# Performance work log

Measured on AMD Instinct MI355X. Metric: run time of the kernel, lower is better.

Reference implementation:

```python
import jax, jax.numpy as jnp
import numpy as np

N = 50000      # n_nodes
E = 800000     # n_edges (avg degree 16)
IN, HID, CLS = 128, 128, 40


def setup_inputs() -> dict:
    key = jax.random.key(0)
    ks = jax.random.split(key, 9)
    features = jax.random.normal(ks[0], (N, IN), dtype=jnp.float32)
    src = jax.random.randint(ks[1], (E,), 0, N)
    dst = jax.random.randint(ks[2], (E,), 0, N)
    # GraphConv weights (glorot-ish scale) and biases
    W0 = jax.random.normal(ks[3], (IN, HID), dtype=jnp.float32) / np.sqrt(IN).astype(np.float32)
    b0 = jnp.zeros((HID,), jnp.float32)
    W1 = jax.random.normal(ks[4], (HID, HID), dtype=jnp.float32) / np.sqrt(HID).astype(np.float32)
    b1 = jnp.zeros((HID,), jnp.float32)
    W2 = jax.random.normal(ks[5], (HID, CLS), dtype=jnp.float32) / np.sqrt(HID).astype(np.float32)
    b2 = jnp.zeros((CLS,), jnp.float32)
    return {"features": features, "src": src, "dst": dst,
            "W0": W0, "b0": b0, "W1": W1, "b1": b1, "W2": W2, "b2": b2}


def _degree_norms(src, dst, dtype):
    # DGL GraphConv norm='both': D_out^{-1/2} on source side, D_in^{-1/2} on dest side,
    # degrees clamped to a minimum of 1.
    ones = jnp.ones(src.shape[0], dtype)
    deg_out = jax.ops.segment_sum(ones, src, num_segments=N)
    deg_in = jax.ops.segment_sum(ones, dst, num_segments=N)
    norm_out = jnp.where(deg_out > 0, deg_out, 1.0) ** -0.5
    norm_in = jnp.where(deg_in > 0, deg_in, 1.0) ** -0.5
    return norm_out, norm_in


def _graph_conv(h, src, dst, norm_out, norm_in, W, b, act):
    # h' = D_in^{-1/2} A D_out^{-1/2} h W + b ; optional relu
    h = (h * norm_out[:, None]) @ W            # dense transform first (in >= out)
    agg = jax.ops.segment_sum(h[src], dst, num_segments=N)  # sparse aggregation
    out = agg * norm_in[:, None] + b
    return jax.nn.relu(out) if act else out


def reference(features, src, dst, W0, b0, W1, b1, W2, b2):
    norm_out, norm_in = _degree_norms(src, dst, features.dtype)
    # dropout is identity in eval mode
    h = _graph_conv(features, src, dst, norm_out, norm_in, W0, b0, True)
    h = _graph_conv(h, src, dst, norm_out, norm_in, W1, b1, True)
    h = _graph_conv(h, src, dst, norm_out, norm_in, W2, b2, False)
    return h
```

## Files before the change

kernel.cpp:

```cpp
#include <hip/hip_runtime.h>
#include <hip/hip_fp16.h>


static constexpr int NN  = 50000;
static constexpr int NE  = 800000;
static constexpr int HID = 128;
static constexpr int CLS = 40;
static constexpr int CAP = 48;

static constexpr int NGEMM  = (NN + 127) / 128;
static constexpr int NBUILD = (NE + 1023) / 1024;
static constexpr int NPREP1 = 8;
static constexpr int NPREP2 = 3;

typedef __attribute__((ext_vector_type(8))) _Float16 f16x8;
typedef __attribute__((ext_vector_type(4))) float    f32x4;
union ABu { uint4 u; f16x8 h; };

__device__ __forceinline__ void gemm128_body(const float* __restrict__ X,
                                             const float* __restrict__ W,
                                             __half* __restrict__ Y,
                                             int tileIdx, float* As, float* Bs) {
    constexpr int BSTR = 132;
    const int tid = threadIdx.x;
    const int rowBase = tileIdx * 128;

    const int bkk = tid >> 3;
    const int bc4 = tid & 7;
    const float* wrow = W + (size_t)bkk * 128 + bc4 * 16;

    const int rt = tid & 15;
    const int ct = tid >> 4;

    float acc[8][8];
    #pragma unroll
    for (int j = 0; j < 8; ++j)
        #pragma unroll
        for (int i = 0; i < 8; ++i) acc[j][i] = 0.f;

    float4 xv[4], wv[4];

    auto loadA = [&](int s) {
        #pragma unroll
        for (int i = 0; i < 4; ++i) {
            int f = tid + 256 * i;
            int r = f >> 3;
            int kc = f & 7;
            int grow = rowBase + r;
            xv[i] = (grow < NN)
                ? *(const float4*)(X + (size_t)grow * 128 + s * 32 + kc * 4)
                : make_float4(0.f, 0.f, 0.f, 0.f);
        }
    };
    auto loadB = [&](int s) {
        const float* p = wrow + (size_t)s * 32 * 128;
        #pragma unroll
        for (int i = 0; i < 4; ++i) wv[i] = ((const float4*)p)[i];
    };
    auto writeLDS = [&]() {
        #pragma unroll
        for (int i = 0; i < 4; ++i) {
            int f = tid + 256 * i;
            int r = f >> 3;
            int kc = f & 7;
            int pc = ((r >> 2) + kc) & 31;
            int base = pc * 4 + (r & 3);
            const float* v = (const float*)&xv[i];
            #pragma unroll
            for (int c = 0; c < 4; ++c)
                As[(kc * 4 + c) * 128 + base] = v[c];
        }
        #pragma unroll
        for (int i = 0; i < 4; ++i)
            *(float4*)&Bs[bkk * BSTR + bc4 * 16 + i * 4] = wv[i];
    };

    loadA(0); loadB(0);
    for (int s = 0; s < 4; ++s) {
        writeLDS();
        __syncthreads();
        if (s < 3) { loadA(s + 1); loadB(s + 1); }
        #pragma unroll 8
        for (int k = 0; k < 32; ++k) {
            int kc = k >> 2;
            int pa0 = (rt + kc) & 31;
            int pa1 = (rt + 16 + kc) & 31;
            float4 a0 = *(const float4*)&As[k * 128 + pa0 * 4];
            float4 a1 = *(const float4*)&As[k * 128 + pa1 * 4];
            float4 b0 = *(const float4*)&Bs[k * BSTR + ct * 8];
            float4 b1 = *(const float4*)&Bs[k * BSTR + ct * 8 + 4];
            float a[8] = {a0.x, a0.y, a0.z, a0.w, a1.x, a1.y, a1.z, a1.w};
            float b[8] = {b0.x, b0.y, b0.z, b0.w, b1.x, b1.y, b1.z, b1.w};
            #pragma unroll
            for (int j = 0; j < 8; ++j)
                #pragma unroll
                for (int ii = 0; ii < 8; ++ii)
                    acc[j][ii] = fmaf(a[j], b[ii], acc[j][ii]);
        }
        __syncthreads();
    }
    union Pack { __half2 h2[4]; uint4 u; };
    #pragma unroll
    for (int j = 0; j < 8; ++j) {
        int row = rowBase + ((j < 4) ? (4 * rt + j) : (64 + 4 * rt + (j - 4)));
        if (row < NN) {
            Pack p;
            #pragma unroll
            for (int q = 0; q < 4; ++q)
                p.h2[q] = __halves2half2(__float2half_rn(acc[j][2 * q]),
                                         __float2half_rn(acc[j][2 * q + 1]));
            *(uint4*)(Y + (size_t)row * 128 + ct * 8) = p.u;
        }
    }
}

__global__ __launch_bounds__(256) void fused_kernel(const float* __restrict__ X,
                                                    const float* __restrict__ W0,
                                                    __half* __restrict__ Y,
                                                    const int* __restrict__ src,
                                                    const int* __restrict__ dst,
                                                    int* __restrict__ deg_out,
                                                    int* __restrict__ cnt,
                                                    unsigned short* __restrict__ colbkt,
                                                    const float* __restrict__ W1,
                                                    __half* __restrict__ W1t,
                                                    const float* __restrict__ W2,
                                                    __half* __restrict__ W2t) {
    __shared__ float As[32 * 128];
    __shared__ float Bs[32 * 132];
    int b = blockIdx.x;
    if (b < NGEMM) {
        gemm128_body(X, W0, Y, b, As, Bs);
    } else if (b < NGEMM + NBUILD) {
        int base = (b - NGEMM) * 1024 + threadIdx.x;
        int e[4], s[4], d[4];
        #pragma unroll
        for (int i = 0; i < 4; ++i) {
            e[i] = base + 256 * i;
            int ec = e[i] < NE ? e[i] : NE - 1;
            s[i] = src[ec];
            d[i] = dst[ec];
        }
        #pragma unroll
        for (int i = 0; i < 4; ++i)
            if (e[i] < NE) atomicAdd(&deg_out[s[i]], 1);
        int slot[4];
        #pragma unroll
        for (int i = 0; i < 4; ++i)
            slot[i] = (e[i] < NE) ? atomicAdd(&cnt[d[i]], 1) : CAP;
        #pragma unroll
        for (int i = 0; i < 4; ++i)
            if (slot[i] < CAP)
                colbkt[(size_t)d[i] * CAP + slot[i]] = (unsigned short)s[i];
    } else if (b < NGEMM + NBUILD + NPREP1) {
        int gid = (b - NGEMM - NBUILD) * 256 + threadIdx.x;
        int n = gid >> 4, q = gid & 15;
        union { __half h[8]; uint4 u; } p;
        #pragma unroll
        for (int j = 0; j < 8; ++j)
            p.h[j] = __float2half_rn(W1[(size_t)(q * 8 + j) * 128 + n]);
        ((uint4*)W1t)[n * 16 + ((q + n) & 15)] = p.u;
    } else {
        int gid = (b - NGEMM - NBUILD - NPREP1) * 256 + threadIdx.x;
        int n = gid >> 4, q = gid & 15;
        union { __half h[8]; uint4 u; } p;
        #pragma unroll
        for (int j = 0; j < 8; ++j)
            p.h[j] = (n < CLS) ? __float2half_rn(W2[(size_t)(q * 8 + j) * CLS + n])
                               : __half(0.f);
        ((uint4*)W2t)[n * 16 + ((q + n) & 15)] = p.u;
    }
}

template <int NT>
__device__ __forceinline__ void mfma_rowgemm_body(const __half* __restrict__ H,
                                                  const float* __restrict__ norm_out,
                                                  __half* __restrict__ Y,
                                                  const __half* Ws) {
    const int tid  = threadIdx.x;
    const int wv   = tid >> 6;
    const int lane = tid & 63;
    const int m    = lane & 15;
    const int quad = lane >> 4;
    const int rowW = blockIdx.x * 64 + wv * 16;

    ABu a[4];
    int arow = rowW + m;
    if (arow >= NN) arow = NN - 1;
    const uint4* hp = (const uint4*)(H + (size_t)arow * 128);
    #pragma unroll
    for (int kc = 0; kc < 4; ++kc)
        a[kc].u = hp[kc * 4 + quad];

    __syncthreads();

    f32x4 acc[NT];
    #pragma unroll
    for (int nt = 0; nt < NT; ++nt) acc[nt] = (f32x4){0.f, 0.f, 0.f, 0.f};

    #pragma unroll
    for (int kc = 0; kc < 4; ++kc) {
        #pragma unroll
        for (int nt = 0; nt < NT; ++nt) {
            int n = nt * 16 + m;
            int q = kc * 4 + quad;
            ABu bf;
            bf.u = ((const uint4*)Ws)[n * 16 + ((q + n) & 15)];
            acc[nt] = __builtin_amdgcn_mfma_f32_16x16x32_f16(a[kc].h, bf.h, acc[nt], 0, 0, 0);
        }
    }

    float nmv[4];
    #pragma unroll
    for (int r = 0; r < 4; ++r) {
        int row = rowW + quad * 4 + r;
        nmv[r] = (row < NN) ? norm_out[row] : 0.f;
    }
    #pragma unroll
    for (int nt = 0; nt < NT; ++nt) {
        int coln = nt * 16 + m;
        #pragma unroll
        for (int r = 0; r < 4; ++r) {
            int row = rowW + quad * 4 + r;
            if (row < NN)
                Y[(size_t)row * (NT * 16) + coln] = __float2half_rn(acc[nt][r] * nmv[r]);
        }
    }
}

__global__ __launch_bounds__(256) void gemm1_mfma(const __half* __restrict__ H,
                                                  const __half* __restrict__ W1t,
                                                  const float* __restrict__ norm_out,
                                                  __half* __restrict__ T) {
    __shared__ __half Ws[128 * 128];
    const int tid = threadIdx.x;
    #pragma unroll
    for (int i = 0; i < 8; ++i)
        ((uint4*)Ws)[tid + 256 * i] = ((const uint4*)W1t)[tid + 256 * i];
    mfma_rowgemm_body<8>(H, norm_out, T, Ws);
}

__global__ __launch_bounds__(256) void gemm40_mfma(const __half* __restrict__ H,
                                                   const __half* __restrict__ W2t,
                                                   const float* __restrict__ norm_out,
                                                   __half* __restrict__ T40) {
    __shared__ __half Ws[48 * 128];
    const int tid = threadIdx.x;
    #pragma unroll
    for (int i = 0; i < 3; ++i)
        ((uint4*)Ws)[tid + 256 * i] = ((const uint4*)W2t)[tid + 256 * i];
    mfma_rowgemm_body<3>(H, norm_out, T40, Ws);
}

__global__ __launch_bounds__(256) void norm_scale_kernel(const int* __restrict__ deg_out,
                                                         const int* __restrict__ cnt,
                                                         float* __restrict__ norm_out,
                                                         float* __restrict__ norm_in,
                                                         __half* __restrict__ t) {
    __shared__ float nms[32];
    int base = blockIdx.x * 32;
    int tid = threadIdx.x;
    if (tid < 32) {
        int v = base + tid;
        float no = 1.f;
        if (v < NN) {
            int dof = deg_out[v], dif = cnt[v];
            no = rsqrtf((float)(dof > 0 ? dof : 1));
            norm_out[v] = no;
            norm_in[v]  = rsqrtf((float)(dif > 0 ? dif : 1));
        }
        nms[tid] = no;
    }
    __syncthreads();
    for (int i = tid; i < 512; i += 256) {
        int ro = i >> 4, ch = i & 15;
        int v = base + ro;
        if (v < NN) {
            uint4* p = (uint4*)t + (size_t)v * 16 + ch;
            uint4 u = *p;
            float nm = nms[ro];
            __half2* hp = (__half2*)&u;
            #pragma unroll
            for (int q = 0; q < 4; ++q) {
                float2 f = __half22float2(hp[q]);
                hp[q] = __halves2half2(__float2half_rn(f.x * nm),
                                       __float2half_rn(f.y * nm));
            }
            *p = u;
        }
    }
}

__global__ __launch_bounds__(256) void agg128h_kernel(const __half* __restrict__ T,
                                                      const unsigned short* __restrict__ colbkt,
                                                      const int* __restrict__ cnt,
                                                      const float* __restrict__ norm_in,
                                                      const float* __restrict__ bias,
                                                      __half* __restrict__ out) {
    const int wv   = threadIdx.x >> 6;
    const int lane = threadIdx.x & 63;
    const int nodeA = blockIdx.x * 8 + wv * 2;
    const int nodeB = nodeA + 1;
    if (nodeA >= NN) return;
    const int grp = lane >> 4;
    const int l16 = lane & 15;

    int dgA = cnt[nodeA]; if (dgA > CAP) dgA = CAP;
    int dgB = (nodeB < NN) ? cnt[nodeB] : 0; if (dgB > CAP) dgB = CAP;
    const unsigned short* bktA = colbkt + (size_t)nodeA * CAP;
    const unsigned short* bktB = colbkt + (size_t)(nodeB < NN ? nodeB : 0) * CAP;

    float accA[8], accB[8];
    #pragma unroll
    for (int i = 0; i < 8; ++i) { accA[i] = 0.f; accB[i] = 0.f; }

    const int dgM = dgA > dgB ? dgA : dgB;
    for (int j = 0; j < dgM; j += 16) {
        uint4 vA[4], vB[4];
        float wA[4], wB[4];
        #pragma unroll
        for (int u = 0; u < 4; ++u) {
            int e   = j + 4 * u + grp;
            int eA  = e < dgA ? e : 0;   wA[u] = e < dgA ? 1.f : 0.f;
            int eB  = e < dgB ? e : 0;   wB[u] = e < dgB ? 1.f : 0.f;
            int sA  = (int)bktA[eA];
            int sB  = (int)bktB[eB];
            vA[u] = ((const uint4*)(T + (size_t)sA * 128))[l16];
            vB[u] = ((const uint4*)(T + (size_t)sB * 128))[l16];
        }
        #pragma unroll
        for (int u = 0; u < 4; ++u) {
            const __half2* ha = (const __half2*)&vA[u];
            const __half2* hb = (const __half2*)&vB[u];
            #pragma unroll
            for (int q = 0; q < 4; ++q) {
                float2 fa = __half22float2(ha[q]);
                float2 fb = __half22float2(hb[q]);
                accA[2 * q]     = fmaf(fa.x, wA[u], accA[2 * q]);
                accA[2 * q + 1] = fmaf(fa.y, wA[u], accA[2 * q + 1]);
                accB[2 * q]     = fmaf(fb.x, wB[u], accB[2 * q]);
                accB[2 * q + 1] = fmaf(fb.y, wB[u], accB[2 * q + 1]);
            }
        }
    }
    #pragma unroll
    for (int i = 0; i < 8; ++i) {
        accA[i] += __shfl_xor(accA[i], 16, 64);
        accA[i] += __shfl_xor(accA[i], 32, 64);
        accB[i] += __shfl_xor(accB[i], 16, 64);
        accB[i] += __shfl_xor(accB[i], 32, 64);
    }
    if (grp < 2) {
        int node = (grp == 0) ? nodeA : nodeB;
        const float* ac = (grp == 0) ? accA : accB;
        if (node < NN) {
            float nm = norm_in[node];
            float4 b0 = ((const float4*)bias)[l16 * 2];
            float4 b1 = ((const float4*)bias)[l16 * 2 + 1];
            float o[8];
            o[0] = fmaf(ac[0], nm, b0.x); o[1] = fmaf(ac[1], nm, b0.y);
            o[2] = fmaf(ac[2], nm, b0.z); o[3] = fmaf(ac[3], nm, b0.w);
            o[4] = fmaf(ac[4], nm, b1.x); o[5] = fmaf(ac[5], nm, b1.y);
            o[6] = fmaf(ac[6], nm, b1.z); o[7] = fmaf(ac[7], nm, b1.w);
            union { __half2 h2[4]; uint4 u; } pk;
            #pragma unroll
            for (int q = 0; q < 4; ++q) {
                float x = fmaxf(o[2 * q], 0.f);
                float y = fmaxf(o[2 * q + 1], 0.f);
                pk.h2[q] = __halves2half2(__float2half_rn(x), __float2half_rn(y));
            }
            ((uint4*)(out + (size_t)node * 128))[l16] = pk.u;
        }
    }
}

__global__ __launch_bounds__(256) void agg40h_kernel(const __half* __restrict__ T,
                                                     const unsigned short* __restrict__ colbkt,
                                                     const int* __restrict__ cnt,
                                                     const float* __restrict__ norm_in,
                                                     const float* __restrict__ bias,
                                                     float* __restrict__ out) {
    int node = blockIdx.x * 4 + (threadIdx.x >> 6);
    int lane = threadIdx.x & 63;
    if (node >= NN) return;
    int dg = cnt[node];
    if (dg > CAP) dg = CAP;
    const unsigned short* bkt = colbkt + (size_t)node * CAP;
    const int g = lane / 6;
    const int c = lane - g * 6;

    float acc[8];
    #pragma unroll
    for (int i = 0; i < 8; ++i) acc[i] = 0.f;

    constexpr int B = 4;
    for (int j = 0; j < dg; j += 8 * B) {
        uint4 v[B];
        float w[B];
        #pragma unroll
        for (int u = 0; u < B; ++u) {
            int e  = j + 8 * u + g;
            bool p = (g < 8) && (e < dg);
            int ec = p ? e : 0;
            int s  = (int)bkt[ec];
            w[u]   = p ? 1.f : 0.f;
            v[u]   = ((const uint4*)(T + (size_t)s * 48))[c];
        }
        #pragma unroll
        for (int u = 0; u < B; ++u) {
            const __half2* hp = (const __half2*)&v[u];
            #pragma unroll
            for (int q = 0; q < 4; ++q) {
                float2 f = __half22float2(hp[q]);
                acc[2 * q]     = fmaf(f.x, w[u], acc[2 * q]);
                acc[2 * q + 1] = fmaf(f.y, w[u], acc[2 * q + 1]);
            }
        }
    }
    #pragma unroll
    for (int i = 0; i < 8; ++i) {
        acc[i] += __shfl(acc[i], lane + 24, 64);
        acc[i] += __shfl(acc[i], lane + 12, 64);
        acc[i] += __shfl(acc[i], lane + 6, 64);
    }
    if (lane < 5) {
        float nm = norm_in[node];
        float4 o0, o1;
        o0.x = fmaf(acc[0], nm, bias[c * 8 + 0]);
        o0.y = fmaf(acc[1], nm, bias[c * 8 + 1]);
        o0.z = fmaf(acc[2], nm, bias[c * 8 + 2]);
        o0.w = fmaf(acc[3], nm, bias[c * 8 + 3]);
        o1.x = fmaf(acc[4], nm, bias[c * 8 + 4]);
        o1.y = fmaf(acc[5], nm, bias[c * 8 + 5]);
        o1.z = fmaf(acc[6], nm, bias[c * 8 + 6]);
        o1.w = fmaf(acc[7], nm, bias[c * 8 + 7]);
        float* op = out + (size_t)node * 40 + c * 8;
        *(float4*)op       = o0;
        *(float4*)(op + 4) = o1;
    }
}

extern "C" void kernel_launch(void* const* d_in, const int* in_sizes, int n_in,
                              void* d_out, int out_size, void* d_ws, size_t ws_size,
                              hipStream_t stream) {
    const float* features = (const float*)d_in[0];
    const int*   src      = (const int*)d_in[1];
    const int*   dst      = (const int*)d_in[2];
    const float* W0       = (const float*)d_in[3];
    const float* b0       = (const float*)d_in[4];
    const float* W1       = (const float*)d_in[5];
    const float* b1       = (const float*)d_in[6];
    const float* W2       = (const float*)d_in[7];
    const float* b2       = (const float*)d_in[8];
    float*       out      = (float*)d_out;

    char* ws = (char*)d_ws;
    auto alloc = [&](size_t bytes) {
        char* p = ws;
        ws += (bytes + 511) & ~(size_t)511;
        return p;
    };
    int*            deg_out  = (int*)alloc((size_t)NN * 4);
    int*            cnt      = (int*)alloc((size_t)NN * 4);
    float*          norm_out = (float*)alloc((size_t)NN * 4);
    float*          norm_in  = (float*)alloc((size_t)NN * 4);
    unsigned short* colbkt   = (unsigned short*)alloc((size_t)NN * CAP * 2);
    __half*         W1t      = (__half*)alloc((size_t)HID * HID * 2);
    __half*         W2t      = (__half*)alloc((size_t)48 * HID * 2);
    __half*         t        = (__half*)alloc((size_t)NN * HID * 2);
    __half*         h        = (__half*)alloc((size_t)NN * HID * 2);
    __half*         t40      = (__half*)alloc((size_t)NN * 48 * 2);
    if ((size_t)(ws - (char*)d_ws) > ws_size) return;

    hipMemsetAsync(deg_out, 0, (size_t)NN * 4, stream);
    hipMemsetAsync(cnt, 0, (size_t)NN * 4, stream);

    int gAgg2  = (NN + 7) / 8;
    int gAgg   = (NN + 3) / 4;
    int gRow64 = (NN + 63) / 64;

    fused_kernel<<<NGEMM + NBUILD + NPREP1 + NPREP2, 256, 0, stream>>>(
        features, W0, t, src, dst, deg_out, cnt, colbkt, W1, W1t, W2, W2t);
    norm_scale_kernel<<<(NN + 31) / 32, 256, 0, stream>>>(deg_out, cnt, norm_out, norm_in, t);

    agg128h_kernel<<<gAgg2, 256, 0, stream>>>(t, colbkt, cnt, norm_in, b0, h);
    gemm1_mfma<<<gRow64, 256, 0, stream>>>(h, W1t, norm_out, t);
    agg128h_kernel<<<gAgg2, 256, 0, stream>>>(t, colbkt, cnt, norm_in, b1, h);
    gemm40_mfma<<<gRow64, 256, 0, stream>>>(h, W2t, norm_out, t40);
    agg40h_kernel<<<gAgg, 256, 0, stream>>>(t40, colbkt, cnt, norm_in, b2, out);
}
```

Baseline: 265.1 us.

## Split 128-wide aggregation into four 32-column phases for cache locality

The 128-feature aggregation kernel is split into four column phases, each launched as its own block range and gathering only a 32-half (64-byte) slice of each source row. The aim is for each phase's working set (50000 rows x 64 B, about 3.2 MB) to stay resident in L2/LLC, so the random neighbour gathers hit cache instead of going to HBM. In exchange, index and count loads are repeated four times, each lane issues one load per iteration instead of four, and the cross-lane reduction needs two extra shuffle stages.

New measurement: 344.5 us. 29.9% more time.

```diff
diff --git a/kernel.cpp b/kernel.cpp
--- a/kernel.cpp
+++ b/kernel.cpp
@@ -12,6 +12,7 @@
 static constexpr int NBUILD = (NE + 1023) / 1024;
 static constexpr int NPREP1 = 8;
 static constexpr int NPREP2 = 3;
+static constexpr int BPP    = (NN + 7) / 8;
 
 typedef __attribute__((ext_vector_type(8))) _Float16 f16x8;
 typedef __attribute__((ext_vector_type(4))) float    f32x4;
@@ -291,24 +292,27 @@
     }
 }
 
-__global__ __launch_bounds__(256) void agg128h_kernel(const __half* __restrict__ T,
+__global__ __launch_bounds__(256) void agg128p_kernel(const __half* __restrict__ T,
                                                       const unsigned short* __restrict__ colbkt,
                                                       const int* __restrict__ cnt,
                                                       const float* __restrict__ norm_in,
                                                       const float* __restrict__ bias,
                                                       __half* __restrict__ out) {
-    const int wv   = threadIdx.x >> 6;
-    const int lane = threadIdx.x & 63;
-    const int nodeA = blockIdx.x * 8 + wv * 2;
+    const int phase = blockIdx.x / BPP;
+    const int bip   = blockIdx.x - phase * BPP;
+    const int wv    = threadIdx.x >> 6;
+    const int lane  = threadIdx.x & 63;
+    const int e     = lane >> 2;
+    const int c     = lane & 3;
+    const int nodeA = (bip * 4 + wv) * 2;
     const int nodeB = nodeA + 1;
     if (nodeA >= NN) return;
-    const int grp = lane >> 4;
-    const int l16 = lane & 15;
 
     int dgA = cnt[nodeA]; if (dgA > CAP) dgA = CAP;
     int dgB = (nodeB < NN) ? cnt[nodeB] : 0; if (dgB > CAP) dgB = CAP;
     const unsigned short* bktA = colbkt + (size_t)nodeA * CAP;
     const unsigned short* bktB = colbkt + (size_t)(nodeB < NN ? nodeB : 0) * CAP;
+    const __half* Tp = T + phase * 32;
 
     float accA[8], accB[8];
     #pragma unroll
@@ -316,47 +320,43 @@
 
     const int dgM = dgA > dgB ? dgA : dgB;
     for (int j = 0; j < dgM; j += 16) {
-        uint4 vA[4], vB[4];
-        float wA[4], wB[4];
-        #pragma unroll
-        for (int u = 0; u < 4; ++u) {
-            int e   = j + 4 * u + grp;
-            int eA  = e < dgA ? e : 0;   wA[u] = e < dgA ? 1.f : 0.f;
-            int eB  = e < dgB ? e : 0;   wB[u] = e < dgB ? 1.f : 0.f;
-            int sA  = (int)bktA[eA];
-            int sB  = (int)bktB[eB];
-            vA[u] = ((const uint4*)(T + (size_t)sA * 128))[l16];
-            vB[u] = ((const uint4*)(T + (size_t)sB * 128))[l16];
-        }
-        #pragma unroll
-        for (int u = 0; u < 4; ++u) {
-            const __half2* ha = (const __half2*)&vA[u];
-            const __half2* hb = (const __half2*)&vB[u];
-            #pragma unroll
-            for (int q = 0; q < 4; ++q) {
-                float2 fa = __half22float2(ha[q]);
-                float2 fb = __half22float2(hb[q]);
-                accA[2 * q]     = fmaf(fa.x, wA[u], accA[2 * q]);
-                accA[2 * q + 1] = fmaf(fa.y, wA[u], accA[2 * q + 1]);
-                accB[2 * q]     = fmaf(fb.x, wB[u], accB[2 * q]);
-                accB[2 * q + 1] = fmaf(fb.y, wB[u], accB[2 * q + 1]);
-            }
+        int ie  = j + e;
+        int eA  = ie < dgA ? ie : 0;   float wA = ie < dgA ? 1.f : 0.f;
+        int eB  = ie < dgB ? ie : 0;   float wB = ie < dgB ? 1.f : 0.f;
+        int sA  = (int)bktA[eA];
+        int sB  = (int)bktB[eB];
+        uint4 vA = ((const uint4*)(Tp + (size_t)sA * 128))[c];
+        uint4 vB = ((const uint4*)(Tp + (size_t)sB * 128))[c];
+        const __half2* ha = (const __half2*)&vA;
+        const __half2* hb = (const __half2*)&vB;
+        #pragma unroll
+        for (int q = 0; q < 4; ++q) {
+            float2 fa = __half22float2(ha[q]);
+            float2 fb = __half22float2(hb[q]);
+            accA[2 * q]     = fmaf(fa.x, wA, accA[2 * q]);
+            accA[2 * q + 1] = fmaf(fa.y, wA, accA[2 * q + 1]);
+            accB[2 * q]     = fmaf(fb.x, wB, accB[2 * q]);
+            accB[2 * q + 1] = fmaf(fb.y, wB, accB[2 * q + 1]);
         }
     }
     #pragma unroll
     for (int i = 0; i < 8; ++i) {
+        accA[i] += __shfl_xor(accA[i], 4, 64);
+        accA[i] += __shfl_xor(accA[i], 8, 64);
         accA[i] += __shfl_xor(accA[i], 16, 64);
         accA[i] += __shfl_xor(accA[i], 32, 64);
+        accB[i] += __shfl_xor(accB[i], 4, 64);
+        accB[i] += __shfl_xor(accB[i], 8, 64);
         accB[i] += __shfl_xor(accB[i], 16, 64);
         accB[i] += __shfl_xor(accB[i], 32, 64);
     }
-    if (grp < 2) {
-        int node = (grp == 0) ? nodeA : nodeB;
-        const float* ac = (grp == 0) ? accA : accB;
+    if (e < 2) {
+        int node = (e == 0) ? nodeA : nodeB;
+        const float* ac = (e == 0) ? accA : accB;
         if (node < NN) {
             float nm = norm_in[node];
-            float4 b0 = ((const float4*)bias)[l16 * 2];
-            float4 b1 = ((const float4*)bias)[l16 * 2 + 1];
+            const float4 b0 = ((const float4*)(bias + phase * 32 + c * 8))[0];
+            const float4 b1 = ((const float4*)(bias + phase * 32 + c * 8))[1];
             float o[8];
             o[0] = fmaf(ac[0], nm, b0.x); o[1] = fmaf(ac[1], nm, b0.y);
             o[2] = fmaf(ac[2], nm, b0.z); o[3] = fmaf(ac[3], nm, b0.w);
@@ -369,7 +369,7 @@
                 float y = fmaxf(o[2 * q + 1], 0.f);
                 pk.h2[q] = __halves2half2(__float2half_rn(x), __float2half_rn(y));
             }
-            ((uint4*)(out + (size_t)node * 128))[l16] = pk.u;
+            ((uint4*)(out + (size_t)node * 128 + phase * 32))[c] = pk.u;
         }
     }
 }
@@ -475,7 +475,7 @@
     hipMemsetAsync(deg_out, 0, (size_t)NN * 4, stream);
     hipMemsetAsync(cnt, 0, (size_t)NN * 4, stream);
 
-    int gAgg2  = (NN + 7) / 8;
+    int gAggP  = 4 * BPP;
     int gAgg   = (NN + 3) / 4;
     int gRow64 = (NN + 63) / 64;
 
@@ -483,9 +483,9 @@
         features, W0, t, src, dst, deg_out, cnt, colbkt, W1, W1t, W2, W2t);
     norm_scale_kernel<<<(NN + 31) / 32, 256, 0, stream>>>(deg_out, cnt, norm_out, norm_in, t);
 
-    agg128h_kernel<<<gAgg2, 256, 0, stream>>>(t, colbkt, cnt, norm_in, b0, h);
+    agg128p_kernel<<<gAggP, 256, 0, stream>>>(t, colbkt, cnt, norm_in, b0, h);
     gemm1_mfma<<<gRow64, 256, 0, stream>>>(h, W1t, norm_out, t);
-    agg128h_kernel<<<gAgg2, 256, 0, stream>>>(t, colbkt, cnt, norm_in, b1, h);
+    agg128p_kernel<<<gAggP, 256, 0, stream>>>(t, colbkt, cnt, norm_in, b1, h);
     gemm40_mfma<<<gRow64, 256, 0, stream>>>(h, W2t, norm_out, t40);
     agg40h_kernel<<<gAgg, 256, 0, stream>>>(t40, colbkt, cnt, norm_in, b2, out);
 }
```
